# Kernel optimization log

Hardware: AMD Instinct MI355X
Metric: run time of the kernel (lower is better)

Reference implementation:

```python
import jax, jax.numpy as jnp
import numpy as np

N = 100000      # num nodes
E = 1600000     # num edges (avg degree 16)
D_IN = 128
D_OUT = 128
EPS = 1e-12     # F.normalize default eps


def setup_inputs() -> dict:
    key = jax.random.key(0)
    k1, k2, k3, k4 = jax.random.split(key, 4)
    x = jax.random.normal(k1, (N, D_IN), dtype=jnp.float32)
    row = jax.random.randint(k2, (E,), 0, N, dtype=jnp.int32)
    # guarantee no self loops in the raw graph: col = (row + offset) % N, offset in [1, N)
    offset = jax.random.randint(k3, (E,), 1, N, dtype=jnp.int32)
    col = (row + offset) % N
    edge_index = jnp.stack([row, col], axis=0)
    # xavier_uniform_ for weight [in, out]
    a = np.sqrt(6.0 / (D_IN + D_OUT)).astype(np.float32)
    weight = jax.random.uniform(k4, (D_IN, D_OUT), dtype=jnp.float32, minval=-a, maxval=a)
    return {"x": x, "edge_index": edge_index, "weight": weight}


def reference(x, edge_index, weight):
    row, col = edge_index[0], edge_index[1]
    # remove_self_loops: drop edges with row == col (mask keeps shapes static)
    mask = (row != col)
    # linear transform first (as in the original forward)
    xw = jnp.matmul(x, weight)                               # [N, D_OUT]
    # scatter_mean over edges with self loops added:
    # out[i] = (sum_{j->i, j!=i} xw[j] + xw[i]) / (deg_nonself(i) + 1)
    msg = jnp.where(mask[:, None], xw[col], jnp.float32(0.0))  # [E, D_OUT]
    seg_sum = jax.ops.segment_sum(msg, row, num_segments=N) + xw
    cnt = jax.ops.segment_sum(mask.astype(xw.dtype), row, num_segments=N) + jnp.float32(1.0)
    out = seg_sum / cnt[:, None]
    # F.normalize(out, p=2, dim=-1): out / max(||out||_2, eps)
    norm = jnp.sqrt(jnp.sum(out * out, axis=-1, keepdims=True))
    out = out / jnp.maximum(norm, jnp.float32(EPS))
    return out
```

## Files before the change

### kernel.cpp

```cpp
#include <hip/hip_runtime.h>
#include <hip/hip_fp16.h>
#include <stdint.h>

#define NN 100000
#define NE 1600000
#define DD 128

#define NBKT 391
#define CAPB 4480
#define NBIN 3125
#define GCAP 1024

typedef _Float16 f16x8 __attribute__((ext_vector_type(8)));
typedef float f32x4 __attribute__((ext_vector_type(4)));

__device__ __forceinline__ uint32_t hadd2u(uint32_t a, uint32_t b){
  union { uint32_t u; __half2 h; } x, y;
  x.u = a; y.u = b;
  x.h = __hadd2(x.h, y.h);
  return x.u;
}
__device__ __forceinline__ uint32_t hmul2u(uint32_t a, __half2 m){
  union { uint32_t u; __half2 h; } x; x.u = a;
  x.h = __hmul2(x.h, m);
  return x.u;
}

__global__ __launch_bounds__(256) void k_part1(
    const int* __restrict__ ei, int* __restrict__ bktres, uint32_t* __restrict__ ibuf,
    const float* __restrict__ w, uint16_t* __restrict__ wsw){
  int b = blockIdx.x, t = threadIdx.x;
  if (b < NBKT){
    __shared__ int sh[NBKT];
    int e0 = b*4096;
    for (int i=t; i<NBKT; i+=256) sh[i] = 0;
    __syncthreads();
    int rr[16], cc[16];
    #pragma unroll
    for (int j=0;j<16;j++){
      int e = e0 + j*256 + t;
      rr[j] = -1;
      if (e < NE){
        rr[j] = ei[e]; cc[j] = ei[NE + e];
        atomicAdd(&sh[rr[j] >> 8], 1);
      }
    }
    __syncthreads();
    for (int i=t; i<NBKT; i+=256){
      int v = sh[i];
      sh[i] = v ? atomicAdd(&bktres[i*16], v) : 0;
    }
    __syncthreads();
    #pragma unroll
    for (int j=0;j<16;j++){
      if (rr[j] >= 0){
        int bk = rr[j] >> 8;
        int p = atomicAdd(&sh[bk], 1);
        if (p < CAPB)
          ibuf[(size_t)bk*CAPB + p] = (uint32_t)(((rr[j] & 255) << 17) | cc[j]);
      }
    }
  } else {
    int wi = (b - NBKT)*256 + t;
    int j = wi & 7, l = (wi >> 3) & 63, kt = (wi >> 9) & 3, ct = wi >> 11;
    int k = kt*32 + ((l >> 4) & 3)*8 + j;
    int d = ct*16 + (l & 15);
    union { _Float16 h; uint16_t u; } cv; cv.h = (_Float16)w[k*DD + d];
    wsw[wi] = cv.u;
  }
}

__global__ __launch_bounds__(256) void k_mid(
    const int* __restrict__ bktres, uint32_t* __restrict__ ibuf,
    uint32_t* __restrict__ rowinfo,
    const float4* __restrict__ x, uint32_t* __restrict__ xs){
  int t = threadIdx.x, b = blockIdx.x;
  if (b >= NBKT){
    int i = (b - NBKT)*256 + t;
    float4 v = x[i];
    union { _Float16 h[4]; uint2 u; } r;
    r.h[0] = (_Float16)v.x; r.h[1] = (_Float16)v.y;
    r.h[2] = (_Float16)v.z; r.h[3] = (_Float16)v.w;
    int n = i >> 5, dq = i & 31;
    uint32_t* dst = xs + (size_t)(dq >> 2)*NN*8 + (size_t)n*8 + (dq & 3)*2;
    *(uint2*)dst = r.u;
    return;
  }
  __shared__ uint32_t s_rec[CAPB];
  __shared__ int s_deg[256], s_off[256], s_cur[256];
  int lane = t & 63, wid = t >> 6;
  int cnt = bktres[b*16]; if (cnt > CAPB) cnt = CAPB;
  size_t bb = (size_t)b*CAPB;
  s_deg[t] = 0;
  __syncthreads();
  for (int i=t; i<cnt; i+=256){
    uint32_t rec = ibuf[bb + i];
    s_rec[i] = rec;
    atomicAdd(&s_deg[rec >> 17], 1);
  }
  __syncthreads();
  if (wid == 0){
    int carry = 0;
    for (int ch=0; ch<4; ch++){
      int idx = ch*64 + lane;
      int o = s_deg[idx], v = o;
      #pragma unroll
      for (int d=1; d<64; d<<=1){ int y = __shfl_up(v, d); if (lane >= d) v += y; }
      int ex = carry + v - o;
      s_off[idx] = ex; s_cur[idx] = ex;
      carry += __shfl(v, 63);
    }
  }
  __syncthreads();
  int dgc = s_deg[t] > 255 ? 255 : s_deg[t];
  rowinfo[b*256 + t] = ((uint32_t)s_off[t] << 8) | (uint32_t)dgc;
  for (int i=t; i<cnt; i+=256){
    uint32_t rec = s_rec[i];
    int p = atomicAdd(&s_cur[rec >> 17], 1);
    ibuf[bb + p] = rec & 0x1FFFFu;
  }
}

__global__ __launch_bounds__(256) void k_gather(
    const uint32_t* __restrict__ xs, const uint32_t* __restrict__ ibuf,
    const uint32_t* __restrict__ rowinfo, uint32_t* __restrict__ aggS){
  __shared__ int s_col[GCAP];
  __shared__ int s_loc[32], s_deg[32];
  int t = threadIdx.x, wid = t >> 6, lane = t & 63;
  int b = blockIdx.x;
  int bin = b >> 3, slice = b & 7;
  int row0 = bin << 5;
  if (t < 32){
    uint32_t info = rowinfo[row0 + t];
    s_loc[t] = (int)(info >> 8);
    s_deg[t] = (int)(info & 255u);
  }
  __syncthreads();
  int base = s_loc[0];
  int len = s_loc[31] + s_deg[31] - base; if (len > GCAP) len = GCAP;
  size_t bb = (size_t)(row0 >> 8)*CAPB + base;
  for (int i=t; i<len; i+=256) s_col[i] = (int)ibuf[bb + i];
  __syncthreads();

  int j = lane >> 3, w = lane & 7;
  int lr = wid*8 + j;
  int r = row0 + lr;
  int dg = s_deg[lr], off = s_loc[lr] - base;
  const uint32_t* xsl = xs + (size_t)slice*NN*8;
  uint32_t acc = 0u;
  int md = dg;
  md = max(md, __shfl_xor(md, 8));
  md = max(md, __shfl_xor(md, 16));
  md = max(md, __shfl_xor(md, 32));
  int s = 0;
  for (; s+4 <= md; s += 4){
    int i0 = off + ((s+0 < dg) ? s+0 : 0);
    int i1 = off + ((s+1 < dg) ? s+1 : 0);
    int i2 = off + ((s+2 < dg) ? s+2 : 0);
    int i3 = off + ((s+3 < dg) ? s+3 : 0);
    int c0 = s_col[i0], c1 = s_col[i1], c2 = s_col[i2], c3 = s_col[i3];
    uint32_t v0 = xsl[(size_t)c0*8 + w];
    uint32_t v1 = xsl[(size_t)c1*8 + w];
    uint32_t v2 = xsl[(size_t)c2*8 + w];
    uint32_t v3 = xsl[(size_t)c3*8 + w];
    if (s+0 < dg) acc = hadd2u(acc, v0);
    if (s+1 < dg) acc = hadd2u(acc, v1);
    if (s+2 < dg) acc = hadd2u(acc, v2);
    if (s+3 < dg) acc = hadd2u(acc, v3);
  }
  for (; s < md; s++){
    int i0 = off + ((s < dg) ? s : 0);
    uint32_t v0 = xsl[(size_t)s_col[i0]*8 + w];
    if (s < dg) acc = hadd2u(acc, v0);
  }
  acc = hadd2u(acc, xsl[(size_t)r*8 + w]);
  acc = hmul2u(acc, __float2half2_rn(1.0f / (float)(dg + 1)));
  aggS[(size_t)slice*NN*8 + (size_t)r*8 + w] = acc;
}

__global__ __launch_bounds__(256) void k_gemm(const uint16_t* __restrict__ agg,
                                              const uint16_t* __restrict__ wsw,
                                              float* __restrict__ out){
  int tid = threadIdx.x, wid = tid >> 6, lane = tid & 63;
  int g = blockIdx.x*4 + wid;
  if (g >= 6250) return;
  const char* aggb = (const char*)agg;
  const f16x8* Bf = (const f16x8*)wsw;
  int row = g*16 + (lane & 15), gk = lane >> 4;
  f16x8 a[4];
  #pragma unroll
  for (int kt=0; kt<4; kt++){
    int d0 = kt*32 + gk*8;
    int slice = d0 >> 4;
    a[kt] = *(const f16x8*)(aggb + (size_t)slice*NN*32 + (size_t)row*32 + ((d0 >> 3) & 1)*16);
  }

  f32x4 acc[8];
  #pragma unroll
  for (int ct=0;ct<8;ct++) acc[ct] = (f32x4){0.f,0.f,0.f,0.f};
  #pragma unroll
  for (int ct=0;ct<8;ct++){
    #pragma unroll
    for (int kt=0;kt<4;kt++)
      acc[ct] = __builtin_amdgcn_mfma_f32_16x16x32_f16(a[kt], Bf[(ct*4+kt)*64 + lane], acc[ct], 0, 0, 0);
  }
  float sq[4] = {0.f,0.f,0.f,0.f};
  #pragma unroll
  for (int ct=0;ct<8;ct++){
    #pragma unroll
    for (int i=0;i<4;i++) sq[i] += acc[ct][i]*acc[ct][i];
  }
  #pragma unroll
  for (int m=1;m<16;m<<=1){
    #pragma unroll
    for (int i=0;i<4;i++) sq[i] += __shfl_xor(sq[i], m);
  }
  float sc4[4];
  #pragma unroll
  for (int i=0;i<4;i++) sc4[i] = 1.0f / fmaxf(sqrtf(sq[i]), 1e-12f);

  int col = lane & 15;
  int rb = g*16 + (gk << 2);
  #pragma unroll
  for (int i=0;i<4;i++){
    int n = rb + i;
    #pragma unroll
    for (int ct=0;ct<8;ct++)
      out[(size_t)n*DD + (ct<<4) + col] = acc[ct][i]*sc4[i];
  }
}

extern "C" void kernel_launch(void* const* d_in, const int* in_sizes, int n_in,
                              void* d_out, int out_size, void* d_ws, size_t ws_size,
                              hipStream_t stream){
  const float* x = (const float*)d_in[0];
  const int*  ei = (const int*)d_in[1];
  const float* w = (const float*)d_in[2];
  float* out = (float*)d_out;
  char* ws = (char*)d_ws;
  (void)in_sizes; (void)n_in; (void)out_size; (void)ws_size;

  size_t off = 0;
  uint32_t* xs  = (uint32_t*)(ws + off); off += (size_t)NN*DD*2;
  uint16_t* agg = (uint16_t*)(ws + off); off += (size_t)NN*DD*2;
  uint16_t* wsw = (uint16_t*)(ws + off); off += (size_t)DD*DD*2;
  uint32_t* ibuf = (uint32_t*)(ws + off); off += (size_t)NBKT*CAPB*4;
  int* bktres   = (int*)(ws + off); off += (size_t)NBKT*16*4;
  uint32_t* rowinfo = (uint32_t*)(ws + off); off += (size_t)NBKT*256*4;

  hipMemsetAsync(bktres, 0, (size_t)NBKT*16*4, stream);
  k_part1<<<NBKT + 64, 256, 0, stream>>>(ei, bktres, ibuf, w, wsw);
  k_mid<<<NBKT + 12500, 256, 0, stream>>>(bktres, ibuf, rowinfo, (const float4*)x, xs);
  k_gather<<<NBIN*8, 256, 0, stream>>>(xs, ibuf, rowinfo, (uint32_t*)agg);
  k_gemm<<<1563, 256, 0, stream>>>(agg, wsw, out);
}
```

Baseline: 146.0 us.

## Widen gather loads to 16B per lane with padded zero row and larger row bins

```diff
diff --git a/kernel.cpp b/kernel.cpp
--- a/kernel.cpp
+++ b/kernel.cpp
@@ -3,13 +3,15 @@
 #include <stdint.h>
 
 #define NN 100000
+#define NNP 100008
 #define NE 1600000
 #define DD 128
 
 #define NBKT 391
 #define CAPB 4480
-#define NBIN 3125
-#define GCAP 1024
+#define NQ 782
+#define QCAP 2944
+#define QLEN 2688
 
 typedef _Float16 f16x8 __attribute__((ext_vector_type(8)));
 typedef float f32x4 __attribute__((ext_vector_type(4)));
@@ -28,7 +30,7 @@
 
 __global__ __launch_bounds__(256) void k_part1(
     const int* __restrict__ ei, int* __restrict__ bktres, uint32_t* __restrict__ ibuf,
-    const float* __restrict__ w, uint16_t* __restrict__ wsw){
+    const float* __restrict__ w, uint16_t* __restrict__ wsw, uint32_t* __restrict__ xs){
   int b = blockIdx.x, t = threadIdx.x;
   if (b < NBKT){
     __shared__ int sh[NBKT];
@@ -60,13 +62,15 @@
           ibuf[(size_t)bk*CAPB + p] = (uint32_t)(((rr[j] & 255) << 17) | cc[j]);
       }
     }
-  } else {
+  } else if (b < NBKT + 64){
     int wi = (b - NBKT)*256 + t;
     int j = wi & 7, l = (wi >> 3) & 63, kt = (wi >> 9) & 3, ct = wi >> 11;
     int k = kt*32 + ((l >> 4) & 3)*8 + j;
     int d = ct*16 + (l & 15);
     union { _Float16 h; uint16_t u; } cv; cv.h = (_Float16)w[k*DD + d];
     wsw[wi] = cv.u;
+  } else {
+    if (t < 64) xs[(size_t)(t >> 3)*NNP*8 + (size_t)NN*8 + (t & 7)] = 0u;
   }
 }
 
@@ -82,7 +86,7 @@
     r.h[0] = (_Float16)v.x; r.h[1] = (_Float16)v.y;
     r.h[2] = (_Float16)v.z; r.h[3] = (_Float16)v.w;
     int n = i >> 5, dq = i & 31;
-    uint32_t* dst = xs + (size_t)(dq >> 2)*NN*8 + (size_t)n*8 + (dq & 3)*2;
+    uint32_t* dst = xs + (size_t)(dq >> 2)*NNP*8 + (size_t)n*8 + (dq & 3)*2;
     *(uint2*)dst = r.u;
     return;
   }
@@ -122,60 +126,58 @@
 }
 
 __global__ __launch_bounds__(256) void k_gather(
-    const uint32_t* __restrict__ xs, const uint32_t* __restrict__ ibuf,
-    const uint32_t* __restrict__ rowinfo, uint32_t* __restrict__ aggS){
-  __shared__ int s_col[GCAP];
-  __shared__ int s_loc[32], s_deg[32];
+    const uint4* __restrict__ xs4, const uint32_t* __restrict__ ibuf,
+    const uint32_t* __restrict__ rowinfo, uint4* __restrict__ agg4){
+  __shared__ int s_col[QCAP];
   int t = threadIdx.x, wid = t >> 6, lane = t & 63;
   int b = blockIdx.x;
-  int bin = b >> 3, slice = b & 7;
-  int row0 = bin << 5;
-  if (t < 32){
-    uint32_t info = rowinfo[row0 + t];
-    s_loc[t] = (int)(info >> 8);
-    s_deg[t] = (int)(info & 255u);
-  }
-  __syncthreads();
-  int base = s_loc[0];
-  int len = s_loc[31] + s_deg[31] - base; if (len > GCAP) len = GCAP;
-  size_t bb = (size_t)(row0 >> 8)*CAPB + base;
+  int q = b >> 3, slice = b & 7;
+  int qrow0 = q << 7;
+  int lastrow = qrow0 + 127; if (lastrow >= NN) lastrow = NN - 1;
+  uint32_t binfo = rowinfo[qrow0];
+  uint32_t linfo = rowinfo[lastrow];
+  int base = (int)(binfo >> 8);
+  int len = (int)(linfo >> 8) + (int)(linfo & 255u) - base;
+  if (len > QLEN) len = QLEN;
+  size_t bb = (size_t)(qrow0 >> 8)*CAPB + base;
   for (int i=t; i<len; i+=256) s_col[i] = (int)ibuf[bb + i];
   __syncthreads();
 
-  int j = lane >> 3, w = lane & 7;
-  int lr = wid*8 + j;
-  int r = row0 + lr;
-  int dg = s_deg[lr], off = s_loc[lr] - base;
-  const uint32_t* xsl = xs + (size_t)slice*NN*8;
-  uint32_t acc = 0u;
+  int r = qrow0 + wid*32 + (lane >> 1);
+  if (r >= NN) return;
+  int w4 = lane & 1;
+  uint32_t info = rowinfo[r];
+  int off = (int)(info >> 8) - base;
+  int dg = (int)(info & 255u);
+  const uint4* xsl = xs4 + (size_t)slice*NNP*2;
+  uint32_t a0 = 0u, a1 = 0u, a2 = 0u, a3 = 0u;
   int md = dg;
+  md = max(md, __shfl_xor(md, 2));
+  md = max(md, __shfl_xor(md, 4));
   md = max(md, __shfl_xor(md, 8));
   md = max(md, __shfl_xor(md, 16));
   md = max(md, __shfl_xor(md, 32));
-  int s = 0;
-  for (; s+4 <= md; s += 4){
-    int i0 = off + ((s+0 < dg) ? s+0 : 0);
-    int i1 = off + ((s+1 < dg) ? s+1 : 0);
-    int i2 = off + ((s+2 < dg) ? s+2 : 0);
-    int i3 = off + ((s+3 < dg) ? s+3 : 0);
-    int c0 = s_col[i0], c1 = s_col[i1], c2 = s_col[i2], c3 = s_col[i3];
-    uint32_t v0 = xsl[(size_t)c0*8 + w];
-    uint32_t v1 = xsl[(size_t)c1*8 + w];
-    uint32_t v2 = xsl[(size_t)c2*8 + w];
-    uint32_t v3 = xsl[(size_t)c3*8 + w];
-    if (s+0 < dg) acc = hadd2u(acc, v0);
-    if (s+1 < dg) acc = hadd2u(acc, v1);
-    if (s+2 < dg) acc = hadd2u(acc, v2);
-    if (s+3 < dg) acc = hadd2u(acc, v3);
-  }
-  for (; s < md; s++){
-    int i0 = off + ((s < dg) ? s : 0);
-    uint32_t v0 = xsl[(size_t)s_col[i0]*8 + w];
-    if (s < dg) acc = hadd2u(acc, v0);
-  }
-  acc = hadd2u(acc, xsl[(size_t)r*8 + w]);
-  acc = hmul2u(acc, __float2half2_rn(1.0f / (float)(dg + 1)));
-  aggS[(size_t)slice*NN*8 + (size_t)r*8 + w] = acc;
+  for (int s = 0; s < md; s += 4){
+    int c0 = (s+0 < dg) ? s_col[off+s+0] : NN;
+    int c1 = (s+1 < dg) ? s_col[off+s+1] : NN;
+    int c2 = (s+2 < dg) ? s_col[off+s+2] : NN;
+    int c3 = (s+3 < dg) ? s_col[off+s+3] : NN;
+    uint4 v0 = xsl[(size_t)c0*2 + w4];
+    uint4 v1 = xsl[(size_t)c1*2 + w4];
+    uint4 v2 = xsl[(size_t)c2*2 + w4];
+    uint4 v3 = xsl[(size_t)c3*2 + w4];
+    a0 = hadd2u(a0, v0.x); a1 = hadd2u(a1, v0.y); a2 = hadd2u(a2, v0.z); a3 = hadd2u(a3, v0.w);
+    a0 = hadd2u(a0, v1.x); a1 = hadd2u(a1, v1.y); a2 = hadd2u(a2, v1.z); a3 = hadd2u(a3, v1.w);
+    a0 = hadd2u(a0, v2.x); a1 = hadd2u(a1, v2.y); a2 = hadd2u(a2, v2.z); a3 = hadd2u(a3, v2.w);
+    a0 = hadd2u(a0, v3.x); a1 = hadd2u(a1, v3.y); a2 = hadd2u(a2, v3.z); a3 = hadd2u(a3, v3.w);
+  }
+  uint4 sv = xsl[(size_t)r*2 + w4];
+  a0 = hadd2u(a0, sv.x); a1 = hadd2u(a1, sv.y); a2 = hadd2u(a2, sv.z); a3 = hadd2u(a3, sv.w);
+  __half2 inv2 = __float2half2_rn(1.0f / (float)(dg + 1));
+  uint4 res;
+  res.x = hmul2u(a0, inv2); res.y = hmul2u(a1, inv2);
+  res.z = hmul2u(a2, inv2); res.w = hmul2u(a3, inv2);
+  agg4[(size_t)slice*NN*2 + (size_t)r*2 + w4] = res;
 }
 
 __global__ __launch_bounds__(256) void k_gemm(const uint16_t* __restrict__ agg,
@@ -241,7 +243,7 @@
   (void)in_sizes; (void)n_in; (void)out_size; (void)ws_size;
 
   size_t off = 0;
-  uint32_t* xs  = (uint32_t*)(ws + off); off += (size_t)NN*DD*2;
+  uint32_t* xs  = (uint32_t*)(ws + off); off += (size_t)NNP*8*32;
   uint16_t* agg = (uint16_t*)(ws + off); off += (size_t)NN*DD*2;
   uint16_t* wsw = (uint16_t*)(ws + off); off += (size_t)DD*DD*2;
   uint32_t* ibuf = (uint32_t*)(ws + off); off += (size_t)NBKT*CAPB*4;
@@ -249,8 +251,8 @@
   uint32_t* rowinfo = (uint32_t*)(ws + off); off += (size_t)NBKT*256*4;
 
   hipMemsetAsync(bktres, 0, (size_t)NBKT*16*4, stream);
-  k_part1<<<NBKT + 64, 256, 0, stream>>>(ei, bktres, ibuf, w, wsw);
+  k_part1<<<NBKT + 65, 256, 0, stream>>>(ei, bktres, ibuf, w, wsw, xs);
   k_mid<<<NBKT + 12500, 256, 0, stream>>>(bktres, ibuf, rowinfo, (const float4*)x, xs);
-  k_gather<<<NBIN*8, 256, 0, stream>>>(xs, ibuf, rowinfo, (uint32_t*)agg);
+  k_gather<<<NQ*8, 256, 0, stream>>>((const uint4*)xs, ibuf, rowinfo, (uint4*)agg);
   k_gemm<<<1563, 256, 0, stream>>>(agg, wsw, out);
 }
```

After: 139.4 us. -4.5%, faster.
